# Kernel tuning notes

Measured on AMD Instinct MI355X. Metric: run time of the kernel, lower is better.

The kernel has to match this reference:

```python
import jax, jax.numpy as jnp
import numpy as np

N = 50000      # nodes (B-rep faces)
E = 800000     # directed edges (avg degree 16)
F_IN = 9       # 8 surface-type flags + is_feature
H1, H2, C = 512, 128, 2


def setup_inputs() -> dict:
    key = jax.random.key(0)
    ks = jax.random.split(key, 8)
    x = jax.random.normal(ks[0], (N, F_IN), dtype=jnp.float32)
    edge_index = jax.random.randint(ks[1], (2, E), 0, N, dtype=jnp.int64)
    W1 = jax.random.normal(ks[2], (F_IN, H1), dtype=jnp.float32) / np.sqrt(F_IN)
    b1 = jnp.zeros((H1,), dtype=jnp.float32)
    W2 = jax.random.normal(ks[3], (H1, H2), dtype=jnp.float32) / np.sqrt(H1)
    b2 = jnp.zeros((H2,), dtype=jnp.float32)
    W3 = jax.random.normal(ks[4], (H2, C), dtype=jnp.float32) / np.sqrt(H2)
    b3 = jnp.zeros((C,), dtype=jnp.float32)
    return {"x": x, "W1": W1, "b1": b1, "W2": W2, "b2": b2,
            "W3": W3, "b3": b3, "edge_index": edge_index}


def reference(x, W1, b1, W2, b2, W3, b3, edge_index):
    n = x.shape[0]
    self_idx = jnp.arange(n, dtype=edge_index.dtype)
    # GCN with self-loops and symmetric normalization (PyG gcn_norm)
    src = jnp.concatenate([edge_index[0], self_idx])  # [E+N]
    dst = jnp.concatenate([edge_index[1], self_idx])  # [E+N]
    deg = jax.ops.segment_sum(jnp.ones_like(src, dtype=x.dtype), dst, num_segments=n)
    dinv = jnp.where(deg > 0, jax.lax.rsqrt(jnp.maximum(deg, 1.0)), 0.0)
    norm = dinv[src] * dinv[dst]  # [E+N]

    def gcn(h, W, b):
        h = h @ W                                   # [N, out]
        msg = h[src] * norm[:, None]                # gather + scale
        return jax.ops.segment_sum(msg, dst, num_segments=n) + b  # scatter-add

    h = jax.nn.relu(gcn(x, W1, b1))
    h = jax.nn.relu(gcn(h, W2, b2))
    # F.dropout with training=False is identity (inference mode)
    h = gcn(h, W3, b3)
    return jax.nn.log_softmax(h, axis=1)
```

## Files before the change

### kernel.cpp

```cpp
#include <hip/hip_runtime.h>
#include <hip/hip_bf16.h>

typedef __attribute__((ext_vector_type(8))) short short8;
typedef __attribute__((ext_vector_type(4))) float float4v;
typedef unsigned int uint;

#define NBLK 192

static __device__ __forceinline__ float2 up_bf2(uint v) {
    float2 r;
    r.x = __uint_as_float(v << 16);
    r.y = __uint_as_float(v & 0xffff0000u);
    return r;
}
static __device__ __forceinline__ short f2bf_bits(float x) {
    union { __hip_bfloat16 h; short s; } u;
    u.h = __float2bfloat16(x);
    return u.s;
}


__global__ __launch_bounds__(256) void k_hist(const int* __restrict__ dst, int E, int chunk,
        int shift, int nbuck, int* __restrict__ histBlk) {
    __shared__ int h[256];
    h[threadIdx.x] = 0;
    __syncthreads();
    int blk = blockIdx.x;
    int e0 = blk * chunk, e1 = min(E, e0 + chunk);
    int nv = (e1 - e0) >> 2;
    const int4* dv = reinterpret_cast<const int4*>(dst + e0);
    for (int i = threadIdx.x; i < nv; i += 256) {
        int4 d = dv[i];
        atomicAdd(&h[d.x >> shift], 1);
        atomicAdd(&h[d.y >> shift], 1);
        atomicAdd(&h[d.z >> shift], 1);
        atomicAdd(&h[d.w >> shift], 1);
    }
    for (int e = e0 + (nv << 2) + threadIdx.x; e < e1; e += 256)
        atomicAdd(&h[dst[e] >> shift], 1);
    __syncthreads();
    if (threadIdx.x < nbuck) histBlk[threadIdx.x * NBLK + blk] = h[threadIdx.x];
}


__global__ __launch_bounds__(256) void k_btot(const int* __restrict__ histBlk,
                                              int* __restrict__ btot) {
    __shared__ int s[256];
    int b = blockIdx.x, t = threadIdx.x;
    s[t] = (t < NBLK) ? histBlk[b * NBLK + t] : 0;
    __syncthreads();
    for (int off = 128; off; off >>= 1) {
        if (t < off) s[t] += s[t + off];
        __syncthreads();
    }
    if (t == 0) btot[b] = s[0];
}


__global__ __launch_bounds__(256) void k_bscan(const int* __restrict__ histBlk,
        const int* __restrict__ btot, int nbuck,
        int* __restrict__ baseBlk, int* __restrict__ bucketBase) {
    __shared__ int s[256], sb[256];
    int b = blockIdx.x, t = threadIdx.x;
    int v = (t < NBLK) ? histBlk[b * NBLK + t] : 0;
    s[t] = v;
    sb[t] = (t < nbuck) ? btot[t] : 0;
    __syncthreads();
    for (int off = 1; off < 256; off <<= 1) {
        int u = (t >= off) ? s[t - off] : 0;
        int u2 = (t >= off) ? sb[t - off] : 0;
        __syncthreads();
        s[t] += u;
        sb[t] += u2;
        __syncthreads();
    }
    int base = (b > 0) ? sb[b - 1] : 0;
    if (t < NBLK) baseBlk[b * NBLK + t] = base + s[t] - v;
    if (t == 0) bucketBase[b] = base;
}


__global__ __launch_bounds__(256) void k_scatterbin(const int* __restrict__ src,
        const int* __restrict__ dst, int E, int chunk, int shift, int nbuck,
        const int* __restrict__ baseBlk, uint* __restrict__ binned) {
    __shared__ int cur[256];
    int blk = blockIdx.x;
    if (threadIdx.x < nbuck) cur[threadIdx.x] = baseBlk[threadIdx.x * NBLK + blk];
    __syncthreads();
    int e0 = blk * chunk, e1 = min(E, e0 + chunk);
    int mask = (1 << shift) - 1;
    int nv = (e1 - e0) >> 2;
    const int4* dv = reinterpret_cast<const int4*>(dst + e0);
    const int4* sv = reinterpret_cast<const int4*>(src + e0);
    for (int i = threadIdx.x; i < nv; i += 256) {
        int4 d = dv[i];
        int4 s = sv[i];
        int p0 = atomicAdd(&cur[d.x >> shift], 1);
        binned[p0] = (uint)s.x | ((uint)(d.x & mask) << 24);
        int p1 = atomicAdd(&cur[d.y >> shift], 1);
        binned[p1] = (uint)s.y | ((uint)(d.y & mask) << 24);
        int p2 = atomicAdd(&cur[d.z >> shift], 1);
        binned[p2] = (uint)s.z | ((uint)(d.z & mask) << 24);
        int p3 = atomicAdd(&cur[d.w >> shift], 1);
        binned[p3] = (uint)s.w | ((uint)(d.w & mask) << 24);
    }
    for (int e = e0 + (nv << 2) + threadIdx.x; e < e1; e += 256) {
        int d = dst[e];
        int pos = atomicAdd(&cur[d >> shift], 1);
        binned[pos] = (uint)src[e] | ((uint)(d & mask) << 24);
    }
}


__global__ __launch_bounds__(256) void k_csrbuild(const uint* __restrict__ binned,
        const int* __restrict__ bucketBase, const float* __restrict__ x,
        int E, int shift, int n, int nbuck,
        int* __restrict__ row_ptr, float* __restrict__ dinv, float* __restrict__ xs,
        int* __restrict__ csr) {
    __shared__ int cnt[256], lcur[256];
    int b = blockIdx.x, t = threadIdx.x;
    cnt[t] = 0;
    __syncthreads();
    int lo = bucketBase[b];
    int hi = (b + 1 < nbuck) ? bucketBase[b + 1] : E;
    for (int e = lo + t; e < hi; e += 256)
        atomicAdd(&cnt[binned[e] >> 24], 1);
    __syncthreads();
    int c = cnt[t];
    lcur[t] = c;
    __syncthreads();
    for (int off = 1; off < 256; off <<= 1) {
        int u = (t >= off) ? lcur[t - off] : 0;
        __syncthreads();
        lcur[t] += u;
        __syncthreads();
    }
    int node0 = b << shift;
    int nodeEnd = min(n, (b + 1) << shift);
    int cntNodes = nodeEnd - node0;
    int myBase = lo + lcur[t] - c;
    if (t < cntNodes) {
        row_ptr[node0 + t] = myBase;
        dinv[node0 + t] = rsqrtf((float)(c + 1));
    }
    if (b == nbuck - 1 && t == 0) row_ptr[n] = E;
    for (int j = t; j < cntNodes * 9; j += 256) {
        int nl = j / 9, f = j - nl * 9;
        float dnl = rsqrtf((float)(cnt[nl] + 1));
        xs[(size_t)(node0 + nl) * 9 + f] = dnl * x[(size_t)(node0 + nl) * 9 + f];
    }
    __syncthreads();
    lcur[t] = myBase;
    __syncthreads();
    for (int e = lo + t; e < hi; e += 256) {
        uint p = binned[e];
        int pos = atomicAdd(&lcur[p >> 24], 1);
        csr[pos] = (int)(p & 0xFFFFFF);
    }
}


__global__ __launch_bounds__(256) void k_agg1w(const float* __restrict__ xs,
                       const float* __restrict__ dinv,
                       const int* __restrict__ row_ptr, const int* __restrict__ csr,
                       const float* __restrict__ W1,
                       __hip_bfloat16* __restrict__ aggx_bf,
                       __hip_bfloat16* __restrict__ W1frag, int n, int nagg) {
    int bid = blockIdx.x;
    if (bid >= nagg) {
        int t = (bid - nagg) * 256 + threadIdx.x;
        if (t < 32 * 64) {
            int ctile = t >> 6, lane = t & 63;
            int col = ctile * 16 + (lane & 15);
            int k0 = (lane >> 4) * 8;
            short8 o;
#pragma unroll
            for (int j = 0; j < 8; ++j) {
                int k = k0 + j;
                o[j] = f2bf_bits(k < 9 ? W1[k * 512 + col] : 0.f);
            }
            *reinterpret_cast<short8*>(W1frag + (size_t)t * 8) = o;
        }
        return;
    }
    int node = bid * 8 + (threadIdx.x >> 5);
    if (node >= n) return;
    int l = threadIdx.x & 31;
    int slot = l >> 4;
    int f = l & 15;
    bool act = f < 9;
    float acc = (act && slot == 0) ? xs[node * 9 + f] : 0.f;
    int e0 = row_ptr[node], e1 = row_ptr[node + 1];
    int e = e0;
    for (; e + 16 <= e1; e += 16) {
        int si[8];
        float xv[8];
#pragma unroll
        for (int j = 0; j < 8; ++j) si[j] = csr[e + 2 * j + slot];
#pragma unroll
        for (int j = 0; j < 8; ++j) xv[j] = act ? xs[si[j] * 9 + f] : 0.f;
#pragma unroll
        for (int j = 0; j < 8; ++j) acc += xv[j];
    }
    for (; e + 4 <= e1; e += 4) {
        int s0 = csr[e + slot], s1 = csr[e + 2 + slot];
        float x0 = act ? xs[s0 * 9 + f] : 0.f;
        float x1 = act ? xs[s1 * 9 + f] : 0.f;
        acc += x0 + x1;
    }
    for (; e + 2 <= e1; e += 2) {
        int s0 = csr[e + slot];
        acc += act ? xs[s0 * 9 + f] : 0.f;
    }
    if (e < e1 && slot == 0) {
        int s0 = csr[e];
        acc += act ? xs[s0 * 9 + f] : 0.f;
    }
    acc += __shfl_xor(acc, 16);
    if (slot == 0) {
        float v = act ? dinv[node] * acc : 0.f;
        __hip_bfloat16* op = aggx_bf + (size_t)node * 32;
        union { __hip_bfloat16 h; short s; } u;
        u.h = __float2bfloat16(v);
        reinterpret_cast<short*>(op)[f] = u.s;
        reinterpret_cast<short*>(op)[16 + f] = 0;
    }
}


__global__ __launch_bounds__(512, 2) void k_l12(const __hip_bfloat16* __restrict__ aggx_bf,
                       const __hip_bfloat16* __restrict__ W1frag, const float* __restrict__ b1,
                       const float* __restrict__ W2, const float* __restrict__ dinv,
                       __hip_bfloat16* __restrict__ t2, int n, int npair) {
    __shared__ short bsh[64 * 128 * 8];
    __shared__ short h1s[8][2][16][40];
    int t = threadIdx.x;

    for (int idx = t; idx < 64 * 128; idx += 512) {
        int kb = idx >> 7, c = idx & 127;
        const float* wp = W2 + (size_t)(kb * 8) * 128 + c;
        short8 o;
#pragma unroll
        for (int j = 0; j < 8; ++j) o[j] = f2bf_bits(wp[j * 128]);
        *reinterpret_cast<short8*>(bsh + (size_t)idx * 8) = o;
    }
    __syncthreads();

    int wid = t >> 6, lane = t & 63;
    int pair = blockIdx.x * 8 + wid;
    if (pair >= npair) return;
    int r = lane & 15, quad = lane >> 4;
    short (*hs0)[40] = h1s[wid][0];
    short (*hs1)[40] = h1s[wid][1];

    int m0 = pair << 5;
    short8 aagg0 = *reinterpret_cast<const short8*>(
        aggx_bf + (size_t)(m0 + r) * 32 + quad * 8);
    short8 aagg1 = *reinterpret_cast<const short8*>(
        aggx_bf + (size_t)(m0 + 16 + r) * 32 + quad * 8);

    float4v acc0[8], acc1[8];
#pragma unroll
    for (int cg = 0; cg < 8; ++cg) {
        acc0[cg] = (float4v){0, 0, 0, 0};
        acc1[cg] = (float4v){0, 0, 0, 0};
    }

    for (int kt = 0; kt < 16; ++kt) {
        short8 bf0 = *reinterpret_cast<const short8*>(
            W1frag + ((size_t)(2 * kt) * 64 + lane) * 8);
        short8 bf1 = *reinterpret_cast<const short8*>(
            W1frag + ((size_t)(2 * kt + 1) * 64 + lane) * 8);
        float4v c00 = __builtin_amdgcn_mfma_f32_16x16x32_bf16(
            aagg0, bf0, (float4v){0, 0, 0, 0}, 0, 0, 0);
        float4v c01 = __builtin_amdgcn_mfma_f32_16x16x32_bf16(
            aagg0, bf1, (float4v){0, 0, 0, 0}, 0, 0, 0);
        float4v c10 = __builtin_amdgcn_mfma_f32_16x16x32_bf16(
            aagg1, bf0, (float4v){0, 0, 0, 0}, 0, 0, 0);
        float4v c11 = __builtin_amdgcn_mfma_f32_16x16x32_bf16(
            aagg1, bf1, (float4v){0, 0, 0, 0}, 0, 0, 0);
        float bb0 = b1[kt * 32 + r];
        float bb1 = b1[kt * 32 + 16 + r];
#pragma unroll
        for (int i = 0; i < 4; ++i) {
            int row = quad * 4 + i;
            hs0[row][r]      = f2bf_bits(fmaxf(c00[i] + bb0, 0.f));
            hs0[row][16 + r] = f2bf_bits(fmaxf(c01[i] + bb1, 0.f));
            hs1[row][r]      = f2bf_bits(fmaxf(c10[i] + bb0, 0.f));
            hs1[row][16 + r] = f2bf_bits(fmaxf(c11[i] + bb1, 0.f));
        }
        short8 am0 = *reinterpret_cast<const short8*>(&hs0[r][quad * 8]);
        short8 am1 = *reinterpret_cast<const short8*>(&hs1[r][quad * 8]);
#pragma unroll
        for (int cg = 0; cg < 8; ++cg) {
            short8 b = *reinterpret_cast<const short8*>(
                bsh + (size_t)(((kt * 4 + quad) * 128) + cg * 16 + r) * 8);
            acc0[cg] = __builtin_amdgcn_mfma_f32_16x16x32_bf16(am0, b, acc0[cg], 0, 0, 0);
            acc1[cg] = __builtin_amdgcn_mfma_f32_16x16x32_bf16(am1, b, acc1[cg], 0, 0, 0);
        }
    }

#pragma unroll
    for (int i = 0; i < 4; ++i) {
        int node0 = m0 + quad * 4 + i;
        if (node0 < n) {
            float di = dinv[node0];
            __hip_bfloat16* op = t2 + (size_t)node0 * 128 + r;
#pragma unroll
            for (int cg = 0; cg < 8; ++cg)
                op[cg * 16] = __float2bfloat16(di * acc0[cg][i]);
        }
        int node1 = m0 + 16 + quad * 4 + i;
        if (node1 < n) {
            float di = dinv[node1];
            __hip_bfloat16* op = t2 + (size_t)node1 * 128 + r;
#pragma unroll
            for (int cg = 0; cg < 8; ++cg)
                op[cg * 16] = __float2bfloat16(di * acc1[cg][i]);
        }
    }
}


__global__ __launch_bounds__(256) void k_agg2(const uint* __restrict__ t2u,
                       const float* __restrict__ dinv,
                       const int* __restrict__ row_ptr, const int* __restrict__ csr,
                       const float* __restrict__ b2, const float* __restrict__ W3,
                       float2* __restrict__ t3, int n) {
    int node = blockIdx.x * 4 + (threadIdx.x >> 6);
    if (node >= n) return;
    int lane = threadIdx.x & 63;
    int half = lane >> 5;
    int cl = lane & 31;
    const uint2* t2v = reinterpret_cast<const uint2*>(t2u);

    float a0 = 0.f, a1 = 0.f, a2 = 0.f, a3 = 0.f;
    if (half == 0) {
        uint2 sv = t2v[(size_t)node * 32 + cl];
        float2 pa = up_bf2(sv.x), pb = up_bf2(sv.y);
        a0 = pa.x; a1 = pa.y; a2 = pb.x; a3 = pb.y;
    }

    int e0 = row_ptr[node], e1 = row_ptr[node + 1];
    int eb = e0;
    for (; eb + 16 <= e1; eb += 16) {
        int si[8];
        uint2 ri[8];
#pragma unroll
        for (int j = 0; j < 8; ++j) si[j] = csr[eb + half + 2 * j];
#pragma unroll
        for (int j = 0; j < 8; ++j) ri[j] = t2v[(size_t)si[j] * 32 + cl];
#pragma unroll
        for (int j = 0; j < 8; ++j) {
            float2 qa = up_bf2(ri[j].x), qb = up_bf2(ri[j].y);
            a0 += qa.x; a1 += qa.y; a2 += qb.x; a3 += qb.y;
        }
    }
    for (; eb + 4 <= e1; eb += 4) {
        int s0 = csr[eb + half], s1 = csr[eb + half + 2];
        uint2 r0 = t2v[(size_t)s0 * 32 + cl];
        uint2 r1 = t2v[(size_t)s1 * 32 + cl];
        float2 qa = up_bf2(r0.x), qb = up_bf2(r0.y);
        float2 qc = up_bf2(r1.x), qd = up_bf2(r1.y);
        a0 += qa.x + qc.x; a1 += qa.y + qc.y;
        a2 += qb.x + qd.x; a3 += qb.y + qd.y;
    }
    for (int e = eb + half; e < e1; e += 2) {
        uint2 rv = t2v[(size_t)csr[e] * 32 + cl];
        float2 qa = up_bf2(rv.x), qb = up_bf2(rv.y);
        a0 += qa.x; a1 += qa.y; a2 += qb.x; a3 += qb.y;
    }

    a0 += __shfl_xor(a0, 32);
    a1 += __shfl_xor(a1, 32);
    a2 += __shfl_xor(a2, 32);
    a3 += __shfl_xor(a3, 32);

    float di = dinv[node];
    float4 bb = *reinterpret_cast<const float4*>(b2 + 4 * cl);
    float h0 = fmaxf(di * a0 + bb.x, 0.f);
    float h1v = fmaxf(di * a1 + bb.y, 0.f);
    float h2 = fmaxf(di * a2 + bb.z, 0.f);
    float h3 = fmaxf(di * a3 + bb.w, 0.f);
    float4 wlo = *reinterpret_cast<const float4*>(W3 + 8 * cl);
    float4 whi = *reinterpret_cast<const float4*>(W3 + 8 * cl + 4);
    float c0 = h0 * wlo.x + h1v * wlo.z + h2 * whi.x + h3 * whi.z;
    float c1 = h0 * wlo.y + h1v * wlo.w + h2 * whi.y + h3 * whi.w;
#pragma unroll
    for (int off = 16; off; off >>= 1) {
        c0 += __shfl_xor(c0, off);
        c1 += __shfl_xor(c1, off);
    }
    if (lane == 0) t3[node] = make_float2(di * c0, di * c1);
}


__global__ void k_agg3(const float2* __restrict__ t3, const float* __restrict__ dinv,
                       const int* __restrict__ row_ptr, const int* __restrict__ csr,
                       const float* __restrict__ b3, float2* __restrict__ outv, int n) {
    int node = blockIdx.x * blockDim.x + threadIdx.x;
    if (node >= n) return;
    float2 s = t3[node];
    float a0 = s.x, a1 = s.y;
    int e0 = row_ptr[node], e1 = row_ptr[node + 1];
    int e = e0;
    for (; e + 4 <= e1; e += 4) {
        int s0 = csr[e], s1 = csr[e + 1], s2 = csr[e + 2], s3 = csr[e + 3];
        float2 q0 = t3[s0], q1 = t3[s1], q2 = t3[s2], q3 = t3[s3];
        a0 += q0.x + q1.x + q2.x + q3.x;
        a1 += q0.y + q1.y + q2.y + q3.y;
    }
    for (; e < e1; ++e) {
        float2 q0 = t3[csr[e]];
        a0 += q0.x;
        a1 += q0.y;
    }
    float di = dinv[node];
    float z0 = di * a0 + b3[0];
    float z1 = di * a1 + b3[1];
    float m = fmaxf(z0, z1);
    float lse = m + logf(expf(z0 - m) + expf(z1 - m));
    outv[node] = make_float2(z0 - lse, z1 - lse);
}


extern "C" void kernel_launch(void* const* d_in, const int* in_sizes, int n_in,
                              void* d_out, int out_size, void* d_ws, size_t ws_size,
                              hipStream_t stream) {
    const float* x  = (const float*)d_in[0];
    const float* W1 = (const float*)d_in[1];
    const float* b1 = (const float*)d_in[2];
    const float* W2 = (const float*)d_in[3];
    const float* b2 = (const float*)d_in[4];
    const float* W3 = (const float*)d_in[5];
    const float* b3 = (const float*)d_in[6];
    const int* edges = (const int*)d_in[7];

    int n = in_sizes[0] / 9;
    int E = in_sizes[7] / 2;
    const int* src = edges;
    const int* dst = edges + E;

    char* p = (char*)d_ws;
    auto alloc = [&](size_t bytes) {
        char* q = p;
        p += (bytes + 511) & ~(size_t)511;
        return q;
    };
    float* dinv       = (float*)alloc((size_t)n * 4);
    int*   row_ptr    = (int*)alloc((size_t)(n + 1) * 4);
    int*   csr        = (int*)alloc((size_t)E * 4);
    int*   histBlk    = (int*)alloc((size_t)256 * NBLK * 4);
    int*   baseBlk    = (int*)alloc((size_t)256 * NBLK * 4);
    int*   btot       = (int*)alloc(256 * 4);
    int*   bucketBase = (int*)alloc(256 * 4);
    uint*  binned     = (uint*)alloc((size_t)E * 4);
    float* xs         = (float*)alloc((size_t)n * 9 * 4);
    __hip_bfloat16* aggx_bf = (__hip_bfloat16*)alloc((size_t)(n + 64) * 32 * 2);
    __hip_bfloat16* W1frag  = (__hip_bfloat16*)alloc((size_t)32 * 64 * 8 * 2);
    __hip_bfloat16* t2 = (__hip_bfloat16*)alloc((size_t)n * 128 * 2);
    float2* t3 = (float2*)alloc((size_t)n * 8);

    const int B = 256;
    int shift = 8;
    int nbuck = ((n - 1) >> shift) + 1;
    int chunk = ((E + NBLK - 1) / NBLK + 3) & ~3;

    k_hist<<<NBLK, B, 0, stream>>>(dst, E, chunk, shift, nbuck, histBlk);
    k_btot<<<nbuck, B, 0, stream>>>(histBlk, btot);
    k_bscan<<<nbuck, B, 0, stream>>>(histBlk, btot, nbuck, baseBlk, bucketBase);
    k_scatterbin<<<NBLK, B, 0, stream>>>(src, dst, E, chunk, shift, nbuck, baseBlk, binned);
    k_csrbuild<<<nbuck, B, 0, stream>>>(binned, bucketBase, x, E, shift, n, nbuck,
                                        row_ptr, dinv, xs, csr);

    int nagg = (n + 7) / 8;
    k_agg1w<<<nagg + 8, B, 0, stream>>>(xs, dinv, row_ptr, csr, W1,
                                        aggx_bf, W1frag, n, nagg);

    int ntile = (n + 15) / 16;
    int npair = (ntile + 1) / 2;
    k_l12<<<(npair + 7) / 8, 512, 0, stream>>>(aggx_bf, W1frag, b1, W2, dinv, t2, n, npair);
    k_agg2<<<(n + 3) / 4, 256, 0, stream>>>((const uint*)t2, dinv, row_ptr, csr, b2, W3, t3, n);

    k_agg3<<<(n + B - 1) / B, B, 0, stream>>>(t3, dinv, row_ptr, csr, b3, (float2*)d_out, n);
}
```

Before: 185.3 us.

## Pad scaled features to 16 floats and vectorize CSR build loads

```diff
diff --git a/kernel.cpp b/kernel.cpp
--- a/kernel.cpp
+++ b/kernel.cpp
@@ -123,8 +123,25 @@
     __syncthreads();
     int lo = bucketBase[b];
     int hi = (b + 1 < nbuck) ? bucketBase[b + 1] : E;
-    for (int e = lo + t; e < hi; e += 256)
-        atomicAdd(&cnt[binned[e] >> 24], 1);
+    if (hi - lo >= 8) {
+        int loA = (lo + 3) & ~3, hiA = hi & ~3;
+        for (int e = lo + t; e < loA; e += 256)
+            atomicAdd(&cnt[binned[e] >> 24], 1);
+        const uint4* bv = reinterpret_cast<const uint4*>(binned + loA);
+        int nv = (hiA - loA) >> 2;
+        for (int i = t; i < nv; i += 256) {
+            uint4 p = bv[i];
+            atomicAdd(&cnt[p.x >> 24], 1);
+            atomicAdd(&cnt[p.y >> 24], 1);
+            atomicAdd(&cnt[p.z >> 24], 1);
+            atomicAdd(&cnt[p.w >> 24], 1);
+        }
+        for (int e = hiA + t; e < hi; e += 256)
+            atomicAdd(&cnt[binned[e] >> 24], 1);
+    } else {
+        for (int e = lo + t; e < hi; e += 256)
+            atomicAdd(&cnt[binned[e] >> 24], 1);
+    }
     __syncthreads();
     int c = cnt[t];
     lcur[t] = c;
@@ -144,18 +161,46 @@
         dinv[node0 + t] = rsqrtf((float)(c + 1));
     }
     if (b == nbuck - 1 && t == 0) row_ptr[n] = E;
-    for (int j = t; j < cntNodes * 9; j += 256) {
-        int nl = j / 9, f = j - nl * 9;
+    for (int j = t; j < cntNodes * 16; j += 256) {
+        int nl = j >> 4, f = j & 15;
         float dnl = rsqrtf((float)(cnt[nl] + 1));
-        xs[(size_t)(node0 + nl) * 9 + f] = dnl * x[(size_t)(node0 + nl) * 9 + f];
+        float val = (f < 9) ? dnl * x[(size_t)(node0 + nl) * 9 + f] : 0.f;
+        xs[(size_t)(node0 + nl) * 16 + f] = val;
     }
     __syncthreads();
     lcur[t] = myBase;
     __syncthreads();
-    for (int e = lo + t; e < hi; e += 256) {
-        uint p = binned[e];
-        int pos = atomicAdd(&lcur[p >> 24], 1);
-        csr[pos] = (int)(p & 0xFFFFFF);
+    if (hi - lo >= 8) {
+        int loA = (lo + 3) & ~3, hiA = hi & ~3;
+        for (int e = lo + t; e < loA; e += 256) {
+            uint p = binned[e];
+            int pos = atomicAdd(&lcur[p >> 24], 1);
+            csr[pos] = (int)(p & 0xFFFFFF);
+        }
+        const uint4* bv = reinterpret_cast<const uint4*>(binned + loA);
+        int nv = (hiA - loA) >> 2;
+        for (int i = t; i < nv; i += 256) {
+            uint4 p = bv[i];
+            int p0 = atomicAdd(&lcur[p.x >> 24], 1);
+            csr[p0] = (int)(p.x & 0xFFFFFF);
+            int p1 = atomicAdd(&lcur[p.y >> 24], 1);
+            csr[p1] = (int)(p.y & 0xFFFFFF);
+            int p2 = atomicAdd(&lcur[p.z >> 24], 1);
+            csr[p2] = (int)(p.z & 0xFFFFFF);
+            int p3 = atomicAdd(&lcur[p.w >> 24], 1);
+            csr[p3] = (int)(p.w & 0xFFFFFF);
+        }
+        for (int e = hiA + t; e < hi; e += 256) {
+            uint p = binned[e];
+            int pos = atomicAdd(&lcur[p >> 24], 1);
+            csr[pos] = (int)(p & 0xFFFFFF);
+        }
+    } else {
+        for (int e = lo + t; e < hi; e += 256) {
+            uint p = binned[e];
+            int pos = atomicAdd(&lcur[p >> 24], 1);
+            csr[pos] = (int)(p & 0xFFFFFF);
+        }
     }
 }
 
@@ -188,8 +233,7 @@
     int l = threadIdx.x & 31;
     int slot = l >> 4;
     int f = l & 15;
-    bool act = f < 9;
-    float acc = (act && slot == 0) ? xs[node * 9 + f] : 0.f;
+    float acc = (slot == 0) ? xs[(size_t)node * 16 + f] : 0.f;
     int e0 = row_ptr[node], e1 = row_ptr[node + 1];
     int e = e0;
     for (; e + 16 <= e1; e += 16) {
@@ -198,27 +242,23 @@
 #pragma unroll
         for (int j = 0; j < 8; ++j) si[j] = csr[e + 2 * j + slot];
 #pragma unroll
-        for (int j = 0; j < 8; ++j) xv[j] = act ? xs[si[j] * 9 + f] : 0.f;
+        for (int j = 0; j < 8; ++j) xv[j] = xs[(size_t)si[j] * 16 + f];
 #pragma unroll
         for (int j = 0; j < 8; ++j) acc += xv[j];
     }
     for (; e + 4 <= e1; e += 4) {
         int s0 = csr[e + slot], s1 = csr[e + 2 + slot];
-        float x0 = act ? xs[s0 * 9 + f] : 0.f;
-        float x1 = act ? xs[s1 * 9 + f] : 0.f;
-        acc += x0 + x1;
+        acc += xs[(size_t)s0 * 16 + f] + xs[(size_t)s1 * 16 + f];
     }
     for (; e + 2 <= e1; e += 2) {
-        int s0 = csr[e + slot];
-        acc += act ? xs[s0 * 9 + f] : 0.f;
+        acc += xs[(size_t)csr[e + slot] * 16 + f];
     }
     if (e < e1 && slot == 0) {
-        int s0 = csr[e];
-        acc += act ? xs[s0 * 9 + f] : 0.f;
+        acc += xs[(size_t)csr[e] * 16 + f];
     }
     acc += __shfl_xor(acc, 16);
     if (slot == 0) {
-        float v = act ? dinv[node] * acc : 0.f;
+        float v = dinv[node] * acc;
         __hip_bfloat16* op = aggx_bf + (size_t)node * 32;
         union { __hip_bfloat16 h; short s; } u;
         u.h = __float2bfloat16(v);
@@ -455,7 +495,7 @@
     int*   btot       = (int*)alloc(256 * 4);
     int*   bucketBase = (int*)alloc(256 * 4);
     uint*  binned     = (uint*)alloc((size_t)E * 4);
-    float* xs         = (float*)alloc((size_t)n * 9 * 4);
+    float* xs         = (float*)alloc((size_t)n * 16 * 4);
     __hip_bfloat16* aggx_bf = (__hip_bfloat16*)alloc((size_t)(n + 64) * 32 * 2);
     __hip_bfloat16* W1frag  = (__hip_bfloat16*)alloc((size_t)32 * 64 * 8 * 2);
     __hip_bfloat16* t2 = (__hip_bfloat16*)alloc((size_t)n * 128 * 2);
```

After: 181.9 us, median of 2. No clear change (-1.8%).
